# Kernel tuning notes

Hardware: AMD Instinct MI355X
Metric: run time of the kernel (lower is better)

Reference implementation:

```python
import jax, jax.numpy as jnp
import numpy as np
from jax import lax

# static config (matches init_kwargs / input_specs)
B, T, DUR = 16, 256, 4
MEL = T * DUR                      # 1024 frames; durations rows each sum to MEL
D, H, DH, L = 512, 8, 64, 4
INTER, K, OUT = 2048, 3, 80
VOCAB, MAXLEN = 256, 4096


def _sincos(maxlen, d):
    den = jnp.exp(-jnp.arange(0, d, 2).astype(jnp.float32) * (np.log(10000.0) / d))
    ang = jnp.arange(maxlen, dtype=jnp.float32)[:, None] * den[None, :]
    return jnp.stack([jnp.sin(ang), jnp.cos(ang)], axis=-1).reshape(maxlen, d)


def _ln(x, g, b):
    m = jnp.mean(x, -1, keepdims=True)
    v = jnp.mean((x - m) ** 2, -1, keepdims=True)
    return (x - m) * lax.rsqrt(v + 1e-5) * g + b


def _layer(x, am, wqkv, bqkv, wo, bo, ln1g, ln1b, c1w, c1b, c2w, c2b, ln2g, ln2b):
    bs, s, _ = x.shape
    qkv = (x @ wqkv + bqkv).reshape(bs, s, 3, H, DH)
    q, k, v = qkv[:, :, 0], qkv[:, :, 1], qkv[:, :, 2]
    scores = jnp.einsum('bqhd,bkhd->bhqk', q, k) / np.sqrt(DH).astype(np.float32)
    scores = scores + am[:, None, None, :]          # additive key mask (-inf padded)
    attn = jax.nn.softmax(scores, axis=-1)
    ctx = jnp.einsum('bhqk,bkhd->bqhd', attn, v).reshape(bs, s, H * DH)
    x = _ln(x + ctx @ wo + bo, ln1g, ln1b)
    h = lax.conv_general_dilated(x, c1w, (1,), 'SAME', dimension_numbers=('NLC', 'LIO', 'NLC')) + c1b
    h = jax.nn.relu(h)
    h = lax.conv_general_dilated(h, c2w, (1,), 'SAME', dimension_numbers=('NLC', 'LIO', 'NLC')) + c2b
    return _ln(x + h, ln2g, ln2b)


def _stack(x, am, params):
    for i in range(L):
        x = _layer(x, am, *(p[i] for p in params))
    return x


def setup_inputs() -> dict:
    key = jax.random.key(0)
    ks = iter(jax.random.split(key, 64))

    def nrm(shape, s=0.02):
        return jax.random.normal(next(ks), shape, jnp.float32) * s

    inp = {
        'tokens': jax.random.randint(next(ks), (B, T), 0, VOCAB),
        'token_lengths': jax.random.randint(next(ks), (B,), T // 2, T),
        'melspec_length': jax.random.randint(next(ks), (B,), MEL // 2, MEL),
        'durations': jnp.full((B, T), DUR, jnp.int32),   # rows sum to MEL (module assert)
        'mel_len': MEL,
        'emb': nrm((VOCAB, D), 1.0),
    }
    for pre in ('enc', 'dec'):
        inp[pre + '_wqkv'] = nrm((L, D, 3 * H * DH))
        inp[pre + '_bqkv'] = jnp.zeros((L, 3 * H * DH))
        inp[pre + '_wo'] = nrm((L, H * DH, D))
        inp[pre + '_bo'] = jnp.zeros((L, D))
        inp[pre + '_ln1g'] = jnp.ones((L, D))
        inp[pre + '_ln1b'] = jnp.zeros((L, D))
        inp[pre + '_c1w'] = nrm((L, K, D, INTER))
        inp[pre + '_c1b'] = jnp.zeros((L, INTER))
        inp[pre + '_c2w'] = nrm((L, K, INTER, D))
        inp[pre + '_c2b'] = jnp.zeros((L, D))
        inp[pre + '_ln2g'] = jnp.ones((L, D))
        inp[pre + '_ln2b'] = jnp.zeros((L, D))
    inp['out_w'] = nrm((D, OUT))
    inp['out_b'] = jnp.zeros((OUT,))
    return inp


def reference(tokens, token_lengths, melspec_length, durations, mel_len, emb,
              enc_wqkv, enc_bqkv, enc_wo, enc_bo, enc_ln1g, enc_ln1b,
              enc_c1w, enc_c1b, enc_c2w, enc_c2b, enc_ln2g, enc_ln2b,
              dec_wqkv, dec_bqkv, dec_wo, dec_bo, dec_ln1g, dec_ln1b,
              dec_c1w, dec_c1b, dec_c2w, dec_c2b, dec_ln2g, dec_ln2b,
              out_w, out_b):
    bs, t = tokens.shape
    pos = _sincos(MAXLEAN := MAXLEN, D)
    x = emb[tokens]
    # faithful to original: x + (x + pos_embedding[:bs]) where pos buffer is [maxlen,1,D]
    x = 2.0 * x + pos[:bs][:, None, :]
    am = jnp.where(jnp.arange(t)[None, :] > token_lengths[:, None], -jnp.inf, 0.0)
    enc = _stack(x, am, (enc_wqkv, enc_bqkv, enc_wo, enc_bo, enc_ln1g, enc_ln1b,
                         enc_c1w, enc_c1b, enc_c2w, enc_c2b, enc_ln2g, enc_ln2b))
    # length regulator: equivalent gather form of mask.T @ encoder (O(MEL*D) not O(T*MEL*D))
    cums = jnp.cumsum(durations, axis=1)
    frames = jnp.arange(mel_len)
    idx = jax.vmap(lambda c: jnp.searchsorted(c, frames, side='right'))(cums)  # [B, MEL]
    dec_in = jnp.take_along_axis(enc, idx[:, :, None], axis=1)
    keep = (frames[None, :] <= melspec_length[:, None]).astype(dec_in.dtype)
    dec_in = dec_in * keep[:, :, None]
    am2 = jnp.where(frames[None, :] > melspec_length[:, None], -jnp.inf, 0.0)
    dec = _stack(dec_in, am2, (dec_wqkv, dec_bqkv, dec_wo, dec_bo, dec_ln1g, dec_ln1b,
                               dec_c1w, dec_c1b, dec_c2w, dec_c2b, dec_ln2g, dec_ln2b))
    out = dec @ out_w + out_b                      # [B, MEL, OUT]
    return jnp.transpose(out, (0, 2, 1))           # [B, OUT, MEL]
```

## Files before the change

### kernel.cpp

```cpp
#include <hip/hip_runtime.h>

typedef unsigned short u16;
typedef short short8 __attribute__((ext_vector_type(8)));
typedef float floatx4 __attribute__((ext_vector_type(4)));

static constexpr int CB = 16, CT = 256, CMEL = 1024, CD = 512, CH = 8, CDH = 64, CL = 4;
static constexpr int CINTER = 2048, COUT = 80;
static constexpr int CQKV = 3 * CH * CDH;

static __device__ __forceinline__ float bf2f(u16 u) {
  union { unsigned u; float f; } v; v.u = ((unsigned)u) << 16; return v.f;
}
static __device__ __forceinline__ u16 f2bf(float f) {
  union { float f; unsigned u; } v; v.f = f;
  unsigned r = v.u + 0x7fffu + ((v.u >> 16) & 1u);
  return (u16)(r >> 16);
}

static __device__ __forceinline__ void gld16(const u16* g, u16* lds) {
  __builtin_amdgcn_global_load_lds((const __attribute__((address_space(1))) void*)g,
                                   (__attribute__((address_space(3))) void*)lds, 16, 0, 0);
}

template<int NT, bool RELU>
__global__ __launch_bounds__(256)
void gemm2_k(const u16* __restrict__ A, const u16* __restrict__ Bm,
             u16* __restrict__ Cm, const float* __restrict__ bias,
             int M, int N, int K, int lda, int ldb, int ldc,
             int Sm1, long tapStrideB, const u16* __restrict__ zp)
{
  constexpr int BM = 128, BN = 128;
  constexpr int H = (NT == 3) ? 8 : 0;
  constexpr int AR = BM + 2 * H;
  __shared__ u16 As[AR * 32];
  __shared__ u16 Bs[NT * BN * 32];

  const int t = threadIdx.x;
  const int lane = t & 63;
  const int wave = t >> 6;
  const int wrow = wave >> 1;
  const int wcol = wave & 1;
  const int bn0 = blockIdx.x * BN;
  const int bm0 = blockIdx.y * BM;

  floatx4 acc[4][4];
#pragma unroll
  for (int i = 0; i < 4; ++i)
#pragma unroll
    for (int j = 0; j < 4; ++j) acc[i][j] = (floatx4){0.f, 0.f, 0.f, 0.f};

  const int rsub = lane >> 2;
  const int g8 = (((lane & 3) ^ ((lane >> 3) & 3)) << 3);

  const u16* aP0; const u16* aP1; const u16* aP2 = nullptr;
  {
    int gg0 = bm0 - H + wave * 16 + rsub;
    int gg1 = bm0 - H + (wave + 4) * 16 + rsub;
    aP0 = ((NT == 1) || ((unsigned)gg0 < (unsigned)M)) ? A + (long)gg0 * lda + g8 : nullptr;
    aP1 = ((NT == 1) || ((unsigned)gg1 < (unsigned)M)) ? A + (long)gg1 * lda + g8 : nullptr;
    if (NT == 3 && wave == 0) {
      int gg2 = bm0 - H + 128 + rsub;
      aP2 = ((unsigned)gg2 < (unsigned)M) ? A + (long)gg2 * lda + g8 : nullptr;
    }
  }
  const int aL0 = wave * 512, aL1 = (wave + 4) * 512, aL2 = 8 * 512;

  const u16* bP[NT][2]; int bL[NT][2];
#pragma unroll
  for (int i = 0; i < NT; ++i)
#pragma unroll
    for (int j = 0; j < 2; ++j) {
      int r = (wave + j * 4) * 16 + rsub;
      bP[i][j] = Bm + (long)i * tapStrideB + (long)(bn0 + r) * ldb + g8;
      bL[i][j] = (i * BN + (wave + j * 4) * 16) * 32;
    }

  const int q = lane >> 4, fm = lane & 15;
  const int swzB = (q ^ ((fm >> 1) & 3)) << 3;
  int swzA[NT];
  bool mv[NT][4];
#pragma unroll
  for (int tap = 0; tap < NT; ++tap) {
    const int dlt = tap - ((NT == 3) ? 1 : 0);
    swzA[tap] = (q ^ ((((H + dlt + fm) & 15) >> 1) & 3)) << 3;
#pragma unroll
    for (int i = 0; i < 4; ++i) {
      int s = (bm0 + wrow * 64 + i * 16 + fm) & Sm1;
      mv[tap][i] = ((unsigned)(s + dlt) <= (unsigned)Sm1);
    }
  }
  const short8 zero8 = {};

  for (int k0 = 0; k0 < K; k0 += 32) {
    gld16(aP0 ? aP0 + k0 : zp, &As[aL0]);
    gld16(aP1 ? aP1 + k0 : zp, &As[aL1]);
    if (NT == 3 && wave == 0) gld16(aP2 ? aP2 + k0 : zp, &As[aL2]);
#pragma unroll
    for (int i = 0; i < NT; ++i)
#pragma unroll
      for (int j = 0; j < 2; ++j) gld16(bP[i][j] + k0, &Bs[bL[i][j]]);
    __syncthreads();

#pragma unroll
    for (int tap = 0; tap < NT; ++tap) {
      const int dlt = tap - ((NT == 3) ? 1 : 0);
      short8 af[4], bfr[4];
#pragma unroll
      for (int i = 0; i < 4; ++i) {
        af[i] = *(const short8*)&As[(wrow * 64 + i * 16 + fm + H + dlt) * 32 + swzA[tap]];
        if (NT == 3 && !mv[tap][i]) af[i] = zero8;
      }
#pragma unroll
      for (int j = 0; j < 4; ++j)
        bfr[j] = *(const short8*)&Bs[(tap * BN + wcol * 64 + j * 16 + fm) * 32 + swzB];
#pragma unroll
      for (int i = 0; i < 4; ++i)
#pragma unroll
        for (int j = 0; j < 4; ++j)
          acc[i][j] = __builtin_amdgcn_mfma_f32_16x16x32_bf16(af[i], bfr[j], acc[i][j], 0, 0, 0);
    }
    __syncthreads();
  }

  const int rbase = bm0 + wrow * 64 + ((lane >> 4) << 2);
  const int cbase = bn0 + wcol * 64 + fm;
#pragma unroll
  for (int j = 0; j < 4; ++j) {
    int col = cbase + j * 16;
    float bv = bias ? bias[col] : 0.f;
#pragma unroll
    for (int i = 0; i < 4; ++i) {
#pragma unroll
      for (int r = 0; r < 4; ++r) {
        int row = rbase + i * 16 + r;
        float v = acc[i][j][r] + bv;
        if (RELU) v = fmaxf(v, 0.f);
        Cm[(long)row * ldc + col] = f2bf(v);
      }
    }
  }
}

__global__ __launch_bounds__(512)
void attn_k(const u16* __restrict__ qkv, const u16* __restrict__ vt,
            u16* __restrict__ ctx, const int* __restrict__ lens, int S)
{
  __shared__ __attribute__((aligned(16))) u16 Ks[2][128 * 32];
  __shared__ __attribute__((aligned(16))) u16 Vts[4][64 * 32];
  __shared__ __attribute__((aligned(16))) u16 Ps[8][16][136];

  const int t = threadIdx.x, lane = t & 63, w = t >> 6;
  const int bh = blockIdx.y, b = bh >> 3, h = bh & 7;
  const int q0 = blockIdx.x * 128;
  const int len = lens[b];
  const int fm = lane & 15, quad = lane >> 4;
  const int swz8 = ((quad ^ ((fm >> 1) & 3)) << 3);
  const int rsub = lane >> 2;
  const int g8 = (((lane & 3) ^ ((lane >> 3) & 3)) << 3);

  const int qrow = q0 + w * 16 + fm;
  short8 bq[2];
  bq[0] = *(const short8*)&qkv[(long)(b * S + qrow) * CQKV + h * 64 + quad * 8];
  bq[1] = *(const short8*)&qkv[(long)(b * S + qrow) * CQKV + h * 64 + 32 + quad * 8];

  const int ksW = w & 1, rgA = w >> 1, rgB = (w >> 1) + 4;
  const u16* kBaseA = qkv + ((long)b * S + rgA * 16 + rsub) * CQKV + CD + h * 64 + ksW * 32 + g8;
  const u16* kBaseB = qkv + ((long)b * S + rgB * 16 + rsub) * CQKV + CD + h * 64 + ksW * 32 + g8;
  u16* kDstA = &Ks[ksW][rgA * 512];
  u16* kDstB = &Ks[ksW][rgB * 512];
  const int kvs0 = (2 * w) >> 2, dhc0 = (2 * w) & 3;
  const int kvs1 = (2 * w + 1) >> 2, dhc1 = (2 * w + 1) & 3;
  const u16* vBase0 = vt + ((long)bh * 64 + dhc0 * 16 + rsub) * S + kvs0 * 32 + g8;
  const u16* vBase1 = vt + ((long)bh * 64 + dhc1 * 16 + rsub) * S + kvs1 * 32 + g8;
  u16* vDst0 = &Vts[kvs0][dhc0 * 512];
  u16* vDst1 = &Vts[kvs1][dhc1 * 512];

  floatx4 acc_o[4];
#pragma unroll
  for (int j = 0; j < 4; ++j) acc_o[j] = (floatx4){0.f, 0.f, 0.f, 0.f};
  float m = -1e30f, l = 0.f;

  for (int kv0 = 0; kv0 < S; kv0 += 128) {
    __syncthreads();
    gld16(kBaseA + (long)kv0 * CQKV, kDstA);
    gld16(kBaseB + (long)kv0 * CQKV, kDstB);
    gld16(vBase0 + kv0, vDst0);
    gld16(vBase1 + kv0, vDst1);
    __syncthreads();

    floatx4 sa[8];
#pragma unroll
    for (int i = 0; i < 8; ++i) sa[i] = (floatx4){0.f, 0.f, 0.f, 0.f};
#pragma unroll
    for (int ks = 0; ks < 2; ++ks) {
#pragma unroll
      for (int mi = 0; mi < 8; ++mi) {
        short8 ak = *(const short8*)&Ks[ks][(mi * 16 + fm) * 32 + swz8];
        sa[mi] = __builtin_amdgcn_mfma_f32_16x16x32_bf16(ak, bq[ks], sa[mi], 0, 0, 0);
      }
    }

    float p[8][4], tm = -1e30f;
#pragma unroll
    for (int mi = 0; mi < 8; ++mi)
#pragma unroll
      for (int r = 0; r < 4; ++r) {
        int kvg = kv0 + mi * 16 + quad * 4 + r;
        float v = (kvg <= len) ? sa[mi][r] * 0.125f : -1e30f;
        p[mi][r] = v; tm = fmaxf(tm, v);
      }
    tm = fmaxf(tm, __shfl_xor(tm, 16));
    tm = fmaxf(tm, __shfl_xor(tm, 32));
    const float mnew = fmaxf(m, tm);
    const float al = __expf(m - mnew);
    float ts = 0.f;
#pragma unroll
    for (int mi = 0; mi < 8; ++mi)
#pragma unroll
      for (int r = 0; r < 4; ++r) { float e = __expf(p[mi][r] - mnew); p[mi][r] = e; ts += e; }
    ts += __shfl_xor(ts, 16);
    ts += __shfl_xor(ts, 32);
    l = l * al + ts; m = mnew;
    float al4[4];
#pragma unroll
    for (int r = 0; r < 4; ++r) al4[r] = __shfl(al, ((lane >> 4) << 2) + r, 64);
#pragma unroll
    for (int j = 0; j < 4; ++j)
#pragma unroll
      for (int r = 0; r < 4; ++r) acc_o[j][r] *= al4[r];

#pragma unroll
    for (int mi = 0; mi < 8; ++mi) {
      unsigned u01 = (unsigned)f2bf(p[mi][0]) | ((unsigned)f2bf(p[mi][1]) << 16);
      unsigned u23 = (unsigned)f2bf(p[mi][2]) | ((unsigned)f2bf(p[mi][3]) << 16);
      *(uint2*)&Ps[w][fm][mi * 16 + quad * 4] = make_uint2(u01, u23);
    }

#pragma unroll
    for (int kvs = 0; kvs < 4; ++kvs) {
      short8 ap = *(const short8*)&Ps[w][fm][kvs * 32 + quad * 8];
#pragma unroll
      for (int nj = 0; nj < 4; ++nj) {
        short8 bv = *(const short8*)&Vts[kvs][(nj * 16 + fm) * 32 + swz8];
        acc_o[nj] = __builtin_amdgcn_mfma_f32_16x16x32_bf16(ap, bv, acc_o[nj], 0, 0, 0);
      }
    }
  }

  float li4[4];
#pragma unroll
  for (int r = 0; r < 4; ++r) li4[r] = 1.f / __shfl(l, ((lane >> 4) << 2) + r, 64);
#pragma unroll
  for (int nj = 0; nj < 4; ++nj)
#pragma unroll
    for (int r = 0; r < 4; ++r) {
      int qr = q0 + w * 16 + quad * 4 + r;
      ctx[(long)(b * S + qr) * CD + h * 64 + nj * 16 + fm] = f2bf(acc_o[nj][r] * li4[r]);
    }
}

template<int BM, int BN>
__global__ __launch_bounds__(256)
void gemmF_k(const u16* __restrict__ A, const u16* __restrict__ Bm,
             float* __restrict__ Cm, const float* __restrict__ bias,
             int M, int N, int K, int lda, int ldb,
             const u16* __restrict__ zp)
{
  __shared__ u16 As[BM * 32];
  __shared__ u16 Bs[BN * 32];

  const int t = threadIdx.x;
  const int lane = t & 63;
  const int wave = t >> 6;
  constexpr int WCOLS = BN / 64;
  const int wrow = wave / WCOLS;
  const int wcol = wave % WCOLS;
  const int bn0 = blockIdx.x * BN;
  const int bm0 = blockIdx.y * BM;

  floatx4 acc[4][4];
#pragma unroll
  for (int i = 0; i < 4; ++i)
#pragma unroll
    for (int j = 0; j < 4; ++j) acc[i][j] = (floatx4){0.f, 0.f, 0.f, 0.f};

  const int rsub = lane >> 2;
  const int g8 = (((lane & 3) ^ ((lane >> 3) & 3)) << 3);
  constexpr int PA = BM / 64, PB = BN / 64;

  const int q = lane >> 4, fm = lane & 15;
  const int swz8 = ((q ^ ((fm >> 1) & 3)) << 3);

  const u16* aP[PA]; const u16* bP[PB];
#pragma unroll
  for (int p = 0; p < PA; ++p)
    aP[p] = A + (long)(bm0 + p * 64 + wave * 16 + rsub) * lda + g8;
#pragma unroll
  for (int p = 0; p < PB; ++p) {
    int r = p * 64 + wave * 16 + rsub;
    bP[p] = ((bn0 + r) < N) ? (Bm + (long)(bn0 + r) * ldb + g8) : nullptr;
  }

  for (int k0 = 0; k0 < K; k0 += 32) {
#pragma unroll
    for (int p = 0; p < PA; ++p)
      gld16(aP[p] + k0, &As[(p * 64 + wave * 16) * 32]);
#pragma unroll
    for (int p = 0; p < PB; ++p)
      gld16(bP[p] ? bP[p] + k0 : zp, &Bs[(p * 64 + wave * 16) * 32]);
    __syncthreads();

    short8 af[4], bfr[4];
#pragma unroll
    for (int i = 0; i < 4; ++i)
      af[i] = *(const short8*)&As[(wrow * 64 + i * 16 + fm) * 32 + swz8];
#pragma unroll
    for (int j = 0; j < 4; ++j)
      bfr[j] = *(const short8*)&Bs[(wcol * 64 + j * 16 + fm) * 32 + swz8];
#pragma unroll
    for (int i = 0; i < 4; ++i)
#pragma unroll
      for (int j = 0; j < 4; ++j)
        acc[i][j] = __builtin_amdgcn_mfma_f32_16x16x32_bf16(af[i], bfr[j], acc[i][j], 0, 0, 0);
    __syncthreads();
  }

  const int rbase = bm0 + wrow * 64 + ((lane >> 4) << 2);
  const int cbase = bn0 + wcol * 64 + (lane & 15);
#pragma unroll
  for (int j = 0; j < 4; ++j) {
    int col = cbase + j * 16;
    if (col >= N) continue;
    float bv = bias ? bias[col] : 0.f;
#pragma unroll
    for (int i = 0; i < 4; ++i) {
#pragma unroll
      for (int r = 0; r < 4; ++r) {
        int row = rbase + i * 16 + r;
        Cm[((long)(row >> 10) * COUT + col) * CMEL + (row & 1023)] = acc[i][j][r] + bv;
      }
    }
  }
}

__global__ void cvt_t_k(const float* __restrict__ src, u16* __restrict__ dst, int K, int N)
{
  const int tap = blockIdx.z;
  const int n0 = blockIdx.x * 32, k0 = blockIdx.y * 32;
  __shared__ float tile[32][33];
  const int t = threadIdx.x;
  const int c = t & 31, rr = t >> 5;
  const float* s = src + (long)tap * K * N;
  u16* d = dst + (long)tap * K * N;
#pragma unroll
  for (int i = 0; i < 4; ++i) {
    int k = k0 + rr + i * 8, n = n0 + c;
    tile[rr + i * 8][c] = (k < K && n < N) ? s[(long)k * N + n] : 0.f;
  }
  __syncthreads();
#pragma unroll
  for (int i = 0; i < 4; ++i) {
    int n = n0 + rr + i * 8, k = k0 + c;
    if (n < N && k < K) d[(long)n * K + k] = f2bf(tile[c][rr + i * 8]);
  }
}

__global__ void vtr_k(const u16* __restrict__ qkv, u16* __restrict__ vt, int S)
{
  const int s0 = blockIdx.x * 64;
  const int bh = blockIdx.y;
  const int b = bh >> 3, h = bh & 7;
  __shared__ u16 tile[64][65];
  const int t = threadIdx.x;
  const int wave = t >> 6, lane = t & 63;
#pragma unroll
  for (int i = 0; i < 16; ++i) {
    int sl = wave * 16 + i;
    tile[sl][lane] = qkv[(long)(b * S + s0 + sl) * CQKV + 2 * CD + h * 64 + lane];
  }
  __syncthreads();
  const int dl = t >> 2, sc4 = (t & 3) << 4;
  u16* dstp = vt + ((long)bh * 64 + dl) * S + s0 + sc4;
  short8 v0, v1;
#pragma unroll
  for (int j = 0; j < 8; ++j) { v0[j] = (short)tile[sc4 + j][dl]; v1[j] = (short)tile[sc4 + 8 + j][dl]; }
  *(short8*)dstp = v0;
  *(short8*)(dstp + 8) = v1;
}

__global__ void fill_k(float* __restrict__ o, int n, float v)
{
  int i = blockIdx.x * 256 + threadIdx.x;
  if (i < n) o[i] = v;
}

__global__ void embed_k(const int* __restrict__ tok, const float* __restrict__ emb,
                        u16* __restrict__ X)
{
  const long idx = (long)blockIdx.x * 256 + threadIdx.x;
  const int d = (int)(idx & (CD - 1));
  const int m = (int)(idx >> 9);
  const int b = m >> 8;
  const float e = emb[(long)tok[m] * CD + d];
  const int i2 = d >> 1;
  const float den = __expf(-(float)(2 * i2) * (9.210340371976184f / 512.f));
  const float ang = (float)b * den;
  const float p = (d & 1) ? __cosf(ang) : __sinf(ang);
  X[idx] = f2bf(2.f * e + p);
}

__global__ void ln_res_k(const u16* __restrict__ X, const u16* __restrict__ Y,
                         const float* __restrict__ g, const float* __restrict__ bta,
                         u16* __restrict__ O)
{
  const int m = blockIdx.x, t = threadIdx.x;
  const long base = (long)m * CD;
  float v0 = bf2f(X[base + t]) + bf2f(Y[base + t]);
  float v1 = bf2f(X[base + t + 256]) + bf2f(Y[base + t + 256]);
  __shared__ float red[256];
  red[t] = v0 + v1; __syncthreads();
  for (int s = 128; s > 0; s >>= 1) { if (t < s) red[t] += red[t + s]; __syncthreads(); }
  const float mean = red[0] * (1.f / 512.f);
  __syncthreads();
  const float d0 = v0 - mean, d1 = v1 - mean;
  red[t] = d0 * d0 + d1 * d1; __syncthreads();
  for (int s = 128; s > 0; s >>= 1) { if (t < s) red[t] += red[t + s]; __syncthreads(); }
  const float rstd = rsqrtf(red[0] * (1.f / 512.f) + 1e-5f);
  O[base + t]       = f2bf(d0 * rstd * g[t] + bta[t]);
  O[base + t + 256] = f2bf(d1 * rstd * g[t + 256] + bta[t + 256]);
}

__global__ void cumsum_k(const int* __restrict__ dur, int* __restrict__ cums)
{
  int b = threadIdx.x;
  if (b < CB) {
    int s = 0;
    for (int t = 0; t < CT; ++t) { s += dur[b * CT + t]; cums[b * CT + t] = s; }
  }
}

__global__ void regulate_k(const u16* __restrict__ xe, const int* __restrict__ cums,
                           const int* __restrict__ mlen, u16* __restrict__ xd)
{
  const int m = blockIdx.x;
  const int b = m >> 10, f = m & (CMEL - 1);
  int lo = 0, hi = CT;
  while (lo < hi) { int mid = (lo + hi) >> 1; if (cums[b * CT + mid] <= f) lo = mid + 1; else hi = mid; }
  const int idx = min(lo, CT - 1);
  const bool keep = (f <= mlen[b]);
  const u16* src = xe + ((long)b * CT + idx) * CD;
  u16* dst = xd + (long)m * CD;
  const int t = threadIdx.x;
  dst[t]       = keep ? src[t] : (u16)0;
  dst[t + 256] = keep ? src[t + 256] : (u16)0;
}

extern "C" void kernel_launch(void* const* d_in, const int* in_sizes, int n_in,
                              void* d_out, int out_size, void* d_ws, size_t ws_size,
                              hipStream_t stream)
{
  (void)in_sizes; (void)n_in;
  const int*   tokens = (const int*)d_in[0];
  const int*   tlen   = (const int*)d_in[1];
  const int*   mlen   = (const int*)d_in[2];
  const int*   dur    = (const int*)d_in[3];
  const float* emb    = (const float*)d_in[5];
  const float* ew[12]; const float* dw[12];
  for (int i = 0; i < 12; ++i) { ew[i] = (const float*)d_in[6 + i]; dw[i] = (const float*)d_in[18 + i]; }
  const float* out_w = (const float*)d_in[30];
  const float* out_b = (const float*)d_in[31];

  const int Me = CB * CT;
  const int Md = CB * CMEL;

  const size_t SZ_ZP   = 256;
  const size_t SZ_WBUF = (size_t)3 * CD * CINTER * 2;
  const size_t SZ_XE   = (size_t)Me * CD * 2;
  const size_t SZ_XD   = (size_t)Md * CD * 2;
  const size_t SZ_QKV  = (size_t)Md * CQKV * 2;
  const size_t SZ_HB   = (size_t)Md * CINTER * 2;
  const size_t SZ_CUMS = (size_t)CB * CT * 4;
  auto al = [](size_t b) { return (b + 255) & ~(size_t)255; };
  size_t U = al(SZ_QKV) > al(SZ_HB) ? al(SZ_QKV) : al(SZ_HB);
  size_t total = al(SZ_ZP) + al(SZ_WBUF) + al(SZ_XE) + 3 * al(SZ_XD) + U + al(SZ_CUMS);
  if (total > ws_size) {
    fill_k<<<dim3((unsigned)((out_size + 255) / 256)), dim3(256), 0, stream>>>(
        (float*)d_out, out_size, 1000.0f);
    return;
  }

  char* p = (char*)d_ws;
  auto take = [&](size_t bytes) { char* r = p; p += al(bytes); return r; };
  u16*  zp   = (u16*)take(SZ_ZP);
  u16*  wbuf = (u16*)take(SZ_WBUF);
  u16*  xe   = (u16*)take(SZ_XE);
  u16*  xd   = (u16*)take(SZ_XD);
  u16*  x1   = (u16*)take(SZ_XD);
  u16*  yb   = (u16*)take(SZ_XD);
  char* U0   = take(U);
  u16*  qkvB = (u16*)U0;
  u16*  hb   = (u16*)U0;
  int* cums = (int*)take(SZ_CUMS);

  hipMemsetAsync(zp, 0, SZ_ZP, stream);

  auto cvtT = [&](const float* s, u16* d, int K, int N, int taps) {
    cvt_t_k<<<dim3((unsigned)((N + 31) / 32), (unsigned)((K + 31) / 32), (unsigned)taps),
              dim3(256), 0, stream>>>(s, d, K, N);
  };

  embed_k<<<dim3((unsigned)((long)Me * CD / 256)), dim3(256), 0, stream>>>(tokens, emb, xe);

  auto run_stack = [&](u16* x, int S, int M, const int* lens, const float* const* W) {
    u16* vt = yb;
    for (int l = 0; l < CL; ++l) {
      cvtT(W[0] + (long)l * CD * CQKV, wbuf, CD, CQKV, 1);
      gemm2_k<1, false><<<dim3(CQKV / 128, M / 128), dim3(256), 0, stream>>>(
          x, wbuf, qkvB, W[1] + l * CQKV, M, CQKV, CD, CD, CD, CQKV, S - 1, 0, zp);
      vtr_k<<<dim3((unsigned)(S / 64), (unsigned)(CB * CH)), dim3(256), 0, stream>>>(qkvB, vt, S);
      attn_k<<<dim3((unsigned)(S / 128), (unsigned)(CB * CH)), dim3(512), 0, stream>>>(
          qkvB, vt, x1, lens, S);
      cvtT(W[2] + (long)l * CD * CD, wbuf, CD, CD, 1);
      gemm2_k<1, false><<<dim3(CD / 128, M / 128), dim3(256), 0, stream>>>(
          x1, wbuf, yb, W[3] + l * CD, M, CD, CD, CD, CD, CD, S - 1, 0, zp);
      ln_res_k<<<dim3((unsigned)M), dim3(256), 0, stream>>>(x, yb, W[4] + l * CD, W[5] + l * CD, x1);
      cvtT(W[6] + (long)l * 3 * CD * CINTER, wbuf, CD, CINTER, 3);
      gemm2_k<3, true><<<dim3(CINTER / 128, M / 128), dim3(256), 0, stream>>>(
          x1, wbuf, hb, W[7] + l * CINTER, M, CINTER, CD, CD, CD, CINTER,
          S - 1, (long)CD * CINTER, zp);
      cvtT(W[8] + (long)l * 3 * CINTER * CD, wbuf, CINTER, CD, 3);
      gemm2_k<3, false><<<dim3(CD / 128, M / 128), dim3(256), 0, stream>>>(
          hb, wbuf, yb, W[9] + l * CD, M, CD, CINTER, CINTER, CINTER, CD,
          S - 1, (long)CINTER * CD, zp);
      ln_res_k<<<dim3((unsigned)M), dim3(256), 0, stream>>>(x1, yb, W[10] + l * CD, W[11] + l * CD, x);
    }
  };

  run_stack(xe, CT, Me, tlen, ew);

  cumsum_k<<<dim3(1), dim3(64), 0, stream>>>(dur, cums);
  regulate_k<<<dim3((unsigned)(CB * CMEL)), dim3(256), 0, stream>>>(xe, cums, mlen, xd);

  run_stack(xd, CMEL, Md, mlen, dw);

  cvtT(out_w, wbuf, CD, COUT, 1);
  gemmF_k<128, 128><<<dim3(1, Md / 128), dim3(256), 0, stream>>>(
      xd, wbuf, (float*)d_out, out_b, Md, COUT, CD, CD, CD, zp);
}
```

Measured before the change: 2.652 ms.

## Add 256x128 double-buffered 8-wave GEMM kernel for large stack GEMMs

Adds gemm8_k, a 512-thread GEMM with a 256x128 tile and double-buffered LDS. It issues the next k-tile's global-to-LDS loads before the MFMAs on the current tile and raises wave priority around the MFMA block. The decoder's projection and conv GEMMs use it, and the first conv GEMM uses it in both stacks. The aim is to hide load latency and raise arithmetic intensity per block. The cost is more LDS per block, fewer blocks on the small encoder grid, and extra barriers per tap.

```diff
diff --git a/kernel.cpp b/kernel.cpp
--- a/kernel.cpp
+++ b/kernel.cpp
@@ -120,6 +120,152 @@
           acc[i][j] = __builtin_amdgcn_mfma_f32_16x16x32_bf16(af[i], bfr[j], acc[i][j], 0, 0, 0);
     }
     __syncthreads();
+  }
+
+  const int rbase = bm0 + wrow * 64 + ((lane >> 4) << 2);
+  const int cbase = bn0 + wcol * 64 + fm;
+#pragma unroll
+  for (int j = 0; j < 4; ++j) {
+    int col = cbase + j * 16;
+    float bv = bias ? bias[col] : 0.f;
+#pragma unroll
+    for (int i = 0; i < 4; ++i) {
+#pragma unroll
+      for (int r = 0; r < 4; ++r) {
+        int row = rbase + i * 16 + r;
+        float v = acc[i][j][r] + bv;
+        if (RELU) v = fmaxf(v, 0.f);
+        Cm[(long)row * ldc + col] = f2bf(v);
+      }
+    }
+  }
+}
+
+template<int NT, bool RELU>
+__global__ __launch_bounds__(512, 2)
+void gemm8_k(const u16* __restrict__ A, const u16* __restrict__ Bm,
+             u16* __restrict__ Cm, const float* __restrict__ bias,
+             int M, int N, int K, int lda, int ldb, int ldc,
+             int Sm1, long tapStrideB, const u16* __restrict__ zp)
+{
+  constexpr int BM = 256, BN = 128;
+  constexpr int H = (NT == 3) ? 8 : 0;
+  constexpr int AR = BM + 2 * H;
+  constexpr int ACH = AR / 16;
+  constexpr int BCH = NT * BN / 16;
+  constexpr int TCH = ACH + BCH;
+  constexpr int MAXS = (TCH + 7) / 8;
+
+  __shared__ __attribute__((aligned(16))) u16 As[2][AR * 32];
+  __shared__ __attribute__((aligned(16))) u16 Bs[2][NT * BN * 32];
+
+  const int t = threadIdx.x;
+  const int lane = t & 63;
+  const int w = t >> 6;
+  const int wrow = w >> 1;
+  const int wcol = w & 1;
+  const int bn0 = blockIdx.x * BN;
+  const int bm0 = blockIdx.y * BM;
+
+  floatx4 acc[4][4];
+#pragma unroll
+  for (int i = 0; i < 4; ++i)
+#pragma unroll
+    for (int j = 0; j < 4; ++j) acc[i][j] = (floatx4){0.f, 0.f, 0.f, 0.f};
+
+  const int rsub = lane >> 2;
+  const int g8 = (((lane & 3) ^ ((lane >> 3) & 3)) << 3);
+
+  const u16* sS[MAXS];
+  int        sOff[MAXS];
+  bool       sIsA[MAXS];
+  bool       sUse[MAXS];
+#pragma unroll
+  for (int s = 0; s < MAXS; ++s) {
+    const int c = w + 8 * s;
+    sUse[s] = (c < TCH);
+    if (c < ACH) {
+      sIsA[s] = true;
+      sOff[s] = c * 512;
+      int gg = bm0 - H + c * 16 + rsub;
+      sS[s] = ((NT == 1) || ((unsigned)gg < (unsigned)M)) ? A + (long)gg * lda + g8 : nullptr;
+    } else {
+      sIsA[s] = false;
+      const int cb = (c - ACH) < BCH ? (c - ACH) : 0;
+      const int tap = cb >> 3, rg = cb & 7;
+      sOff[s] = (tap * BN + rg * 16) * 32;
+      sS[s] = Bm + (long)tap * tapStrideB + (long)(bn0 + rg * 16 + rsub) * ldb + g8;
+    }
+  }
+
+  const int q = lane >> 4, fm = lane & 15;
+  const int swzB = (q ^ ((fm >> 1) & 3)) << 3;
+  int swzA[NT];
+  bool mv[NT][4];
+#pragma unroll
+  for (int tap = 0; tap < NT; ++tap) {
+    const int dlt = tap - ((NT == 3) ? 1 : 0);
+    swzA[tap] = (q ^ ((((H + dlt + fm) & 15) >> 1) & 3)) << 3;
+#pragma unroll
+    for (int i = 0; i < 4; ++i) {
+      int sq = (bm0 + wrow * 64 + i * 16 + fm) & Sm1;
+      mv[tap][i] = ((unsigned)(sq + dlt) <= (unsigned)Sm1);
+    }
+  }
+  const short8 zero8 = {};
+
+  auto tile = [&](int k0, const u16* Ard, const u16* Brd,
+                  u16* Awr, u16* Bwr, bool doStage) {
+    if (doStage) {
+      const int k1 = k0 + 32;
+#pragma unroll
+      for (int s = 0; s < MAXS; ++s)
+        if (sUse[s]) {
+          u16* dst = (sIsA[s] ? Awr : Bwr) + sOff[s];
+          gld16(sS[s] ? sS[s] + k1 : zp, dst);
+        }
+    }
+#pragma unroll
+    for (int tap = 0; tap < NT; ++tap) {
+      const int dlt = tap - ((NT == 3) ? 1 : 0);
+      short8 af[4], bfr[4];
+#pragma unroll
+      for (int i = 0; i < 4; ++i) {
+        af[i] = *(const short8*)&Ard[(wrow * 64 + i * 16 + fm + H + dlt) * 32 + swzA[tap]];
+        if (NT == 3 && !mv[tap][i]) af[i] = zero8;
+      }
+#pragma unroll
+      for (int j = 0; j < 4; ++j)
+        bfr[j] = *(const short8*)&Brd[(tap * BN + wcol * 64 + j * 16 + fm) * 32 + swzB];
+      __builtin_amdgcn_s_barrier();
+      asm volatile("s_waitcnt lgkmcnt(0)" ::: "memory");
+      __builtin_amdgcn_sched_barrier(0);
+      __builtin_amdgcn_s_setprio(1);
+#pragma unroll
+      for (int i = 0; i < 4; ++i)
+#pragma unroll
+        for (int j = 0; j < 4; ++j)
+          acc[i][j] = __builtin_amdgcn_mfma_f32_16x16x32_bf16(af[i], bfr[j], acc[i][j], 0, 0, 0);
+      __builtin_amdgcn_s_setprio(0);
+      if (tap == NT - 1)
+        asm volatile("s_waitcnt vmcnt(0)" ::: "memory");
+      __builtin_amdgcn_s_barrier();
+    }
+  };
+
+#pragma unroll
+  for (int s = 0; s < MAXS; ++s)
+    if (sUse[s]) {
+      u16* dst = (sIsA[s] ? &As[0][0] : &Bs[0][0]) + sOff[s];
+      gld16(sS[s] ? sS[s] : zp, dst);
+    }
+  asm volatile("s_waitcnt vmcnt(0)" ::: "memory");
+  __builtin_amdgcn_s_barrier();
+
+  const int ntiles = K >> 5;
+  for (int tt = 0; tt < ntiles; tt += 2) {
+    tile(tt * 32,      &As[0][0], &Bs[0][0], &As[1][0], &Bs[1][0], tt + 1 < ntiles);
+    tile(tt * 32 + 32, &As[1][0], &Bs[1][0], &As[0][0], &Bs[0][0], tt + 2 < ntiles);
   }
 
   const int rbase = bm0 + wrow * 64 + ((lane >> 4) << 2);
@@ -513,25 +659,39 @@
 
   auto run_stack = [&](u16* x, int S, int M, const int* lens, const float* const* W) {
     u16* vt = yb;
+    const bool big = (M >= 8192);
     for (int l = 0; l < CL; ++l) {
       cvtT(W[0] + (long)l * CD * CQKV, wbuf, CD, CQKV, 1);
-      gemm2_k<1, false><<<dim3(CQKV / 128, M / 128), dim3(256), 0, stream>>>(
-          x, wbuf, qkvB, W[1] + l * CQKV, M, CQKV, CD, CD, CD, CQKV, S - 1, 0, zp);
+      if (big)
+        gemm8_k<1, false><<<dim3(CQKV / 128, M / 256), dim3(512), 0, stream>>>(
+            x, wbuf, qkvB, W[1] + l * CQKV, M, CQKV, CD, CD, CD, CQKV, S - 1, 0, zp);
+      else
+        gemm2_k<1, false><<<dim3(CQKV / 128, M / 128), dim3(256), 0, stream>>>(
+            x, wbuf, qkvB, W[1] + l * CQKV, M, CQKV, CD, CD, CD, CQKV, S - 1, 0, zp);
       vtr_k<<<dim3((unsigned)(S / 64), (unsigned)(CB * CH)), dim3(256), 0, stream>>>(qkvB, vt, S);
       attn_k<<<dim3((unsigned)(S / 128), (unsigned)(CB * CH)), dim3(512), 0, stream>>>(
           qkvB, vt, x1, lens, S);
       cvtT(W[2] + (long)l * CD * CD, wbuf, CD, CD, 1);
-      gemm2_k<1, false><<<dim3(CD / 128, M / 128), dim3(256), 0, stream>>>(
-          x1, wbuf, yb, W[3] + l * CD, M, CD, CD, CD, CD, CD, S - 1, 0, zp);
+      if (big)
+        gemm8_k<1, false><<<dim3(CD / 128, M / 256), dim3(512), 0, stream>>>(
+            x1, wbuf, yb, W[3] + l * CD, M, CD, CD, CD, CD, CD, S - 1, 0, zp);
+      else
+        gemm2_k<1, false><<<dim3(CD / 128, M / 128), dim3(256), 0, stream>>>(
+            x1, wbuf, yb, W[3] + l * CD, M, CD, CD, CD, CD, CD, S - 1, 0, zp);
       ln_res_k<<<dim3((unsigned)M), dim3(256), 0, stream>>>(x, yb, W[4] + l * CD, W[5] + l * CD, x1);
       cvtT(W[6] + (long)l * 3 * CD * CINTER, wbuf, CD, CINTER, 3);
-      gemm2_k<3, true><<<dim3(CINTER / 128, M / 128), dim3(256), 0, stream>>>(
+      gemm8_k<3, true><<<dim3(CINTER / 128, M / 256), dim3(512), 0, stream>>>(
           x1, wbuf, hb, W[7] + l * CINTER, M, CINTER, CD, CD, CD, CINTER,
           S - 1, (long)CD * CINTER, zp);
       cvtT(W[8] + (long)l * 3 * CINTER * CD, wbuf, CINTER, CD, 3);
-      gemm2_k<3, false><<<dim3(CD / 128, M / 128), dim3(256), 0, stream>>>(
-          hb, wbuf, yb, W[9] + l * CD, M, CD, CINTER, CINTER, CINTER, CD,
-          S - 1, (long)CINTER * CD, zp);
+      if (big)
+        gemm8_k<3, false><<<dim3(CD / 128, M / 256), dim3(512), 0, stream>>>(
+            hb, wbuf, yb, W[9] + l * CD, M, CD, CINTER, CINTER, CINTER, CD,
+            S - 1, (long)CINTER * CD, zp);
+      else
+        gemm2_k<3, false><<<dim3(CD / 128, M / 128), dim3(256), 0, stream>>>(
+            hb, wbuf, yb, W[9] + l * CD, M, CD, CINTER, CINTER, CINTER, CD,
+            S - 1, (long)CINTER * CD, zp);
       ln_res_k<<<dim3((unsigned)M), dim3(256), 0, stream>>>(x1, yb, W[10] + l * CD, W[11] + l * CD, x);
     }
   };
```

New measurement: 3.111 ms. +17.3%, slower.
